# Optimization experiments

Measured on AMD Instinct MI355X. Metric: run time of the kernel, lower is better.

The kernel has to match this reference:

```python
import jax, jax.numpy as jnp
import numpy as np

N_NODES = 16
N_EDGES = 64
N_LAYERS = 4


def _gcn(x, src, dst, emask, W, b):
    # PyG GCNConv: add self-loops, symmetric deg^-1/2 normalization, sum-aggregate.
    n = x.shape[0]
    h = x @ W  # [n, d_out]
    deg = jax.ops.segment_sum(emask, dst, num_segments=n) + 1.0  # +1 self-loop
    dinv = jax.lax.rsqrt(deg)
    norm = dinv[src] * dinv[dst] * emask  # masked-out edges get 0 weight
    out = jax.ops.segment_sum(norm[:, None] * h[src], dst, num_segments=n)
    return out + (dinv * dinv)[:, None] * h + b  # self-loop term + bias


def _sag_pool(x, src, dst, emask, w_rel, b_rel, w_root, k):
    # SAGPooling with GraphConv scorer: score = lin_rel(sum_j x_j) + lin_root(x)
    n = x.shape[0]
    agg = jax.ops.segment_sum(emask[:, None] * x[src], dst, num_segments=n)
    score = agg @ w_rel + b_rel + x @ w_root  # [n]
    perm = jnp.argsort(-score)[:k]  # top-k nodes
    x_new = x[perm] * jnp.tanh(score[perm])[:, None]
    kept = jnp.zeros(n, bool).at[perm].set(True)
    pos = jnp.zeros(n, jnp.int32).at[perm].set(jnp.arange(k, dtype=jnp.int32))
    emask_new = emask * kept[src] * kept[dst]  # drop edges touching removed nodes
    return x_new, pos[src], pos[dst], emask_new


def _conv_gnn(x, src, dst, W0, Ws, bs, pWrel, pbrel, pWroot, linW, linb):
    emask = jnp.ones(src.shape[0], x.dtype)
    n = x.shape[0]
    for i in range(N_LAYERS):
        W = W0 if i == 0 else Ws[i - 1]
        x = jax.nn.relu(_gcn(x, src, dst, emask, W, bs[i]))
        k = -(-n // 2)  # ceil(0.5 * n) -- SAGPooling ratio=0.5
        x, src, dst, emask = _sag_pool(x, src, dst, emask, pWrel[i], pbrel[i], pWroot[i], k)
        n = k
    x = x @ linW + linb  # [1, 128]
    return jax.nn.log_softmax(x, axis=1)


def _fc(h, fcW, fcb, lnw, lnb):
    eps = 1e-5
    for i in range(3):
        h = h @ fcW[i] + fcb[i]
        mu = h.mean(-1, keepdims=True)
        var = ((h - mu) ** 2).mean(-1, keepdims=True)
        h = (h - mu) * jax.lax.rsqrt(var + eps) * lnw[i] + lnb[i]
        h = jax.nn.relu(h)
    return h @ fcW[3] + fcb[3]


def setup_inputs() -> dict:
    key = jax.random.key(0)
    ks = iter(jax.random.split(key, 64))

    def rn(shape, s=0.05):
        return jax.random.normal(next(ks), shape, jnp.float32) * s

    def gnn_params(p):
        return {
            p + '_W0': rn((45, 128)), p + '_W': rn((3, 128, 128)),
            p + '_b': jnp.zeros((4, 128), jnp.float32),
            p + '_pWrel': rn((4, 128)), p + '_pbrel': jnp.zeros((4,), jnp.float32),
            p + '_pWroot': rn((4, 128)),
            p + '_linW': rn((128, 128)), p + '_linb': jnp.zeros((128,), jnp.float32),
        }

    inp = {
        'gp_x': rn((N_NODES, 45), 1.0), 'sp_x': rn((N_NODES, 45), 1.0),
        'gp_src': jax.random.randint(next(ks), (N_EDGES,), 0, N_NODES, jnp.int32),
        'gp_dst': jax.random.randint(next(ks), (N_EDGES,), 0, N_NODES, jnp.int32),
        'sp_src': jax.random.randint(next(ks), (N_EDGES,), 0, N_NODES, jnp.int32),
        'sp_dst': jax.random.randint(next(ks), (N_EDGES,), 0, N_NODES, jnp.int32),
        'fcW': rn((4, 256, 256)), 'fcb': jnp.zeros((4, 256), jnp.float32),
        'lnw': jnp.ones((3, 256), jnp.float32), 'lnb': jnp.zeros((3, 256), jnp.float32),
    }
    inp.update(gnn_params('g'))
    inp.update(gnn_params('s'))
    return inp


def reference(gp_x, sp_x, gp_src, gp_dst, sp_src, sp_dst,
              g_W0, g_W, g_b, g_pWrel, g_pbrel, g_pWroot, g_linW, g_linb,
              s_W0, s_W, s_b, s_pWrel, s_pbrel, s_pWroot, s_linW, s_linb,
              fcW, fcb, lnw, lnb):
    out1 = _conv_gnn(gp_x, gp_src, gp_dst, g_W0, g_W, g_b, g_pWrel, g_pbrel, g_pWroot, g_linW, g_linb)
    out2 = _conv_gnn(sp_x, sp_src, sp_dst, s_W0, s_W, s_b, s_pWrel, s_pbrel, s_pWroot, s_linW, s_linb)
    concat = jnp.concatenate((out1.reshape(-1), out2.reshape(-1)))  # [256]
    return _fc(concat, fcW, fcb, lnw, lnb)
```

## Files before the change

### kernel.cpp

```cpp
#include <hip/hip_runtime.h>
#include <math.h>

#define MAGIC 0x5F3759DFu
typedef unsigned int u32;

__device__ __forceinline__ void bar_lds(){
  asm volatile("s_waitcnt lgkmcnt(0)\n\ts_barrier" ::: "memory");
}
__device__ __forceinline__ void bar_vm0(){
  asm volatile("s_waitcnt vmcnt(0) lgkmcnt(0)\n\ts_barrier" ::: "memory");
}
__device__ __forceinline__ void bar_vm8(){
  asm volatile("s_waitcnt vmcnt(8) lgkmcnt(0)\n\ts_barrier" ::: "memory");
}

__device__ inline float wsum(float v){
  #pragma unroll
  for (int o=32;o;o>>=1) v += __shfl_xor(v,o,64);
  return v;
}
__device__ inline float wmax(float v){
  #pragma unroll
  for (int o=32;o;o>>=1) v = fmaxf(v,__shfl_xor(v,o,64));
  return v;
}
__device__ inline float hsum32(float v){
  #pragma unroll
  for (int o=16;o;o>>=1) v += __shfl_xor(v,o,64);
  return v;
}
__device__ __forceinline__ void stageW(const float* g, float* l, int nfloats,
                                       int wid, int lane){
  const int nch = nfloats>>8;
  for (int c=wid; c<nch; c+=8)
    __builtin_amdgcn_global_load_lds(
      (__attribute__((address_space(1))) u32*)(void*)(g+(c<<8)+(lane<<2)),
      (__attribute__((address_space(3))) u32*)(void*)(l+(c<<8)), 16, 0, 0);
}
__device__ __forceinline__ void pf(const float* p, int nfloats, int tid){
  float4 acc={0.f,0.f,0.f,0.f};
  const int nq=nfloats>>2;
  for (int i=tid;i<nq;i+=512){
    const float4 v=((const float4*)p)[i];
    acc.x+=v.x; acc.y+=v.y; acc.z+=v.z; acc.w+=v.w;
  }
  asm volatile("" :: "v"(acc.x),"v"(acc.y),"v"(acc.z),"v"(acc.w));
}
__device__ __forceinline__ void poll1(const u32* f, int lane){
  u32 v=0;
  do {
    if (lane==0) v=__hip_atomic_load(f,__ATOMIC_ACQUIRE,__HIP_MEMORY_SCOPE_AGENT);
    v=(u32)__shfl((int)v,0,64);
    if (v!=MAGIC) __builtin_amdgcn_s_sleep(1);
  } while (v!=MAGIC);
}
__device__ __forceinline__ float aload(const float* p){
  return __hip_atomic_load(p,__ATOMIC_RELAXED,__HIP_MEMORY_SCOPE_AGENT);
}
__device__ __forceinline__ void astore(float* p, float v){
  __hip_atomic_store(p,v,__ATOMIC_RELAXED,__HIP_MEMORY_SCOPE_AGENT);
}

template<int F,int VH,int N>
__device__ __forceinline__ void cmain2(int lt, const float* slot,
                                       const float* ZBp, float* PBp){
  constexpr int CH = 128/F;
  const int c4 = lt&31, r = lt>>5;
  const int fh = r & (F-1), vh = r / F;
  const int f0 = fh*CH;
  const float4* slot4 = (const float4*)slot;
  float4 acc[VH];
  #pragma unroll
  for (int i=0;i<VH;++i) acc[i]=make_float4(0.f,0.f,0.f,0.f);
  #pragma unroll
  for (int f=0; f<CH; ++f){
    const float4 w4 = slot4[(f0+f)*32 + c4];
    #pragma unroll
    for (int i=0;i<VH;++i){
      const float zv = ZBp[((vh*VH+i)<<7) + f0 + f];
      acc[i].x+=zv*w4.x; acc[i].y+=zv*w4.y; acc[i].z+=zv*w4.z; acc[i].w+=zv*w4.w;
    }
  }
  #pragma unroll
  for (int i=0;i<VH;++i){
    acc[i].x+=__shfl_xor(acc[i].x,32,64);
    acc[i].y+=__shfl_xor(acc[i].y,32,64);
    acc[i].z+=__shfl_xor(acc[i].z,32,64);
    acc[i].w+=__shfl_xor(acc[i].w,32,64);
  }
  if (!(r&1)){
    const int fp = fh>>1;
    float4* P4=(float4*)PBp;
    #pragma unroll
    for (int i=0;i<VH;++i)
      P4[(fp*N + vh*VH + i)*32 + c4] = acc[i];
  }
}

__global__ __launch_bounds__(512,1) void net_kernel(
    const float* __restrict__ gp_x, const float* __restrict__ sp_x,
    const int* __restrict__ gp_src, const int* __restrict__ gp_dst,
    const int* __restrict__ sp_src, const int* __restrict__ sp_dst,
    const float* __restrict__ g_W0, const float* __restrict__ g_W,
    const float* __restrict__ g_b,  const float* __restrict__ g_pWrel,
    const float* __restrict__ g_pbrel, const float* __restrict__ g_pWroot,
    const float* __restrict__ g_linW, const float* __restrict__ g_linb,
    const float* __restrict__ s_W0, const float* __restrict__ s_W,
    const float* __restrict__ s_b,  const float* __restrict__ s_pWrel,
    const float* __restrict__ s_pbrel, const float* __restrict__ s_pWroot,
    const float* __restrict__ s_linW, const float* __restrict__ s_linb,
    const float* __restrict__ fcW, const float* __restrict__ fcb,
    const float* __restrict__ lnw, const float* __restrict__ lnb,
    float* __restrict__ wsbuf, float* __restrict__ out)
{
  __shared__ __align__(16) float slotA[16384];
  __shared__ __align__(16) float slotB[16384];
  __shared__ __align__(16) float XBx[16][128];
  __shared__ __align__(16) float ZBraw[1024];
  __shared__ __align__(16) float PBf[2048];
  __shared__ __align__(16) float wrelL[512], wrootL[512];
  __shared__ __align__(16) float Adn[256], Mdn[256];
  __shared__ float d1P[64], d2P[64];
  __shared__ float yA[128];
  __shared__ float tsA[8]; __shared__ int permA[8];
  __shared__ float fcin[256]; __shared__ float wpart[16];
  __shared__ int   cntL[16];

  const int lt  = threadIdx.x;
  const int bid = blockIdx.x;
  const int wid = lt>>6, lane = lt&63;
  const int qfc = (wid<<3)+(lane&7);

  if (bid >= 5){
    if (bid==5){ pf(g_W0,5760,lt); pf(g_pWrel,512,lt); pf(g_pWroot,512,lt);
                 pf(g_b,512,lt);   pf(g_linb,128,lt); }
    else if (bid==6){ pf(s_W0,5760,lt); pf(s_pWrel,512,lt); pf(s_pWroot,512,lt);
                 pf(s_b,512,lt);   pf(s_linb,128,lt); }
    else if (bid<=10) pf(g_W + (bid-7)*12288, 12288, lt);
    else if (bid<=14) pf(s_W + (bid-11)*12288, 12288, lt);
    else if (bid<=16) pf(g_linW + (bid-15)*8192, 8192, lt);
    else              pf(s_linW + (bid-17)*8192, 8192, lt);
    return;
  }

  if (bid >= 2){
    const int L = bid-1;
    const int f0fc=(lane>>3)<<5;
    float4 wr[32];
    #pragma unroll
    for (int t=0;t<32;++t) wr[t]=*(const float4*)(fcW+(L<<16)+(f0fc+t)*256+(qfc<<2));
    const float4 bb=*(const float4*)(fcb+(L<<8)+(qfc<<2));
    float4 lw={0,0,0,0}, lb2={0,0,0,0};
    if (L<3){ lw=*(const float4*)(lnw+(L<<8)+(qfc<<2)); lb2=*(const float4*)(lnb+(L<<8)+(qfc<<2)); }

    float zr[32];
    if (bid==2){
      float b0=0.f,w0=0.f,l0=0.f;
      if (lt<256){ b0=fcb[lt]; w0=lnw[lt]; l0=lnb[lt]; }
      poll1((const u32*)(wsbuf+256), lane);
      poll1((const u32*)(wsbuf+576), lane);
      float h=0.f;
      if (lt<256){
        h = aload(wsbuf+lt) + aload(wsbuf+320+lt) + b0;
        float s=wsum(h), s2=wsum(h*h);
        if (lane==0){ wpart[wid]=s; wpart[8+wid]=s2; }
      }
      bar_lds();
      if (lt<256){
        const float S =wpart[0]+wpart[1]+wpart[2]+wpart[3];
        const float S2=wpart[8]+wpart[9]+wpart[10]+wpart[11];
        const float mu=S*(1.f/256.f);
        const float ri=rsqrtf(S2*(1.f/256.f)-mu*mu+1e-5f);
        fcin[lt]=fmaxf((h-mu)*ri*w0+l0,0.f);
      }
      bar_lds();
      #pragma unroll
      for (int t=0;t<32;++t) zr[t]=fcin[f0fc+t];
    } else {
      const int floff = (bid==3)?896:1216;
      const int srcoff= (bid==3)?640:960;
      poll1((const u32*)(wsbuf+floff), lane);
      #pragma unroll
      for (int t=0;t<32;++t) zr[t]=aload(wsbuf+srcoff+f0fc+t);
    }
    float4 a={0.f,0.f,0.f,0.f};
    #pragma unroll
    for (int t=0;t<32;++t){
      a.x+=zr[t]*wr[t].x; a.y+=zr[t]*wr[t].y; a.z+=zr[t]*wr[t].z; a.w+=zr[t]*wr[t].w;
    }
    #pragma unroll
    for (int m=8;m<64;m<<=1){
      a.x+=__shfl_xor(a.x,m,64); a.y+=__shfl_xor(a.y,m,64);
      a.z+=__shfl_xor(a.z,m,64); a.w+=__shfl_xor(a.w,m,64);
    }
    if (bid==4){
      if (lane<8){
        float4 r; r.x=a.x+bb.x; r.y=a.y+bb.y; r.z=a.z+bb.z; r.w=a.w+bb.w;
        *(float4*)(out+(qfc<<2))=r;
      }
      return;
    }
    const bool act=(lane<8);
    float4 hv={0.f,0.f,0.f,0.f};
    if (act){
      hv.x=a.x+bb.x; hv.y=a.y+bb.y; hv.z=a.z+bb.z; hv.w=a.w+bb.w;
      float s=hv.x+hv.y+hv.z+hv.w;
      float s2=hv.x*hv.x+hv.y*hv.y+hv.z*hv.z+hv.w*hv.w;
      #pragma unroll
      for (int m=1;m<8;m<<=1){ s+=__shfl_xor(s,m,64); s2+=__shfl_xor(s2,m,64); }
      if (lane==0){ wpart[wid]=s; wpart[8+wid]=s2; }
    }
    bar_lds();
    if (act){
      float S=0.f,S2=0.f;
      #pragma unroll
      for (int w2=0;w2<8;++w2){ S+=wpart[w2]; S2+=wpart[8+w2]; }
      const float mu=S*(1.f/256.f);
      const float ri=rsqrtf(S2*(1.f/256.f)-mu*mu+1e-5f);
      float* dst=wsbuf + ((bid==2)?640:960) + (qfc<<2);
      astore(dst+0,fmaxf((hv.x-mu)*ri*lw.x+lb2.x,0.f));
      astore(dst+1,fmaxf((hv.y-mu)*ri*lw.y+lb2.y,0.f));
      astore(dst+2,fmaxf((hv.z-mu)*ri*lw.z+lb2.z,0.f));
      astore(dst+3,fmaxf((hv.w-mu)*ri*lw.w+lb2.w,0.f));
    }
    bar_vm0();
    if (lt==0) __hip_atomic_store((u32*)(wsbuf+((bid==2)?896:1216)),MAGIC,__ATOMIC_RELEASE,__HIP_MEMORY_SCOPE_AGENT);
    return;
  }

  const int br = bid;
  const float* x0    = br ? sp_x    : gp_x;
  const int*   srcg  = br ? sp_src  : gp_src;
  const int*   dstg  = br ? sp_dst  : gp_dst;
  const float* W0    = br ? s_W0    : g_W0;
  const float* Wl    = br ? s_W     : g_W;
  const float* bl    = br ? s_b     : g_b;
  const float* wrel  = br ? s_pWrel : g_pWrel;
  const float* brel  = br ? s_pbrel : g_pbrel;
  const float* wroot = br ? s_pWroot: g_pWroot;
  const float* linWg = br ? s_linW  : g_linW;
  const float* linb  = br ? s_linb  : g_linb;
  float* wsOut = wsbuf + br*320;
  u32*   wsFlag = (u32*)(wsbuf + 256 + br*320);
  const int f0fc=(lane>>3)<<4;

  float xv[4];
  #pragma unroll
  for (int r=0;r<4;++r){
    const int i=lt+(r<<9), v=i>>7, f=i&127;
    xv[r] = (f<45)? x0[v*45+f] : 0.f;
  }
  int es=0, ed=0; float emk=0.f;
  if (lt<64){ es=srcg[lt]; ed=dstg[lt]; emk=1.f; }
  const float4 brelv = *(const float4*)brel;
  const int bi4=(lt&31)<<2;
  const float4 blv0=*(const float4*)(bl       + bi4);
  const float4 blv1=*(const float4*)(bl + 128 + bi4);
  const float4 blv2=*(const float4*)(bl + 256 + bi4);
  const float4 blv3=*(const float4*)(bl + 384 + bi4);
  const float linb_s = linb[lt>>2];
  asm volatile("" ::: "memory");
  stageW(wrel,  wrelL,  512, wid, lane);
  stageW(wroot, wrootL, 512, wid, lane);
  stageW(Wl,    slotA, 16384, wid, lane);

  auto build_dense=[&](int kk, float wlane, bool with_ts){
    const float4 z4={0.f,0.f,0.f,0.f};
    *(float4*)&Adn[lt<<2]=z4;
    *(float4*)&Mdn[lt<<2]=z4;
    if (lt<16) cntL[lt]=0;
    const bool act=(emk!=0.f);
    if (act) atomicAdd(&cntL[ed],1);
    const float dinvl = (lt<16)? rsqrtf(1.f+(float)cntL[lt]) : 0.f;
    const float dvs=__shfl(dinvl,es,64);
    const float dvd=__shfl(dinvl,ed,64);
    if (act){
      atomicAdd(&Adn[ed*16+es], dvs*dvd*wlane);
      atomicAdd(&Mdn[ed*16+es], 1.f);
    }
    if (lt<kk){
      const float tv = with_ts ? tsA[lt] : 1.f;
      atomicAdd(&Adn[lt*17], dinvl*dinvl*tv);
    }
  };
  auto doE=[&](int n,int k,float bv,bool rebuild){
    if (lt<64){
      float sc=-INFINITY;
      if (lt<n){
        float acc=d2P[lt<<2]+bv;
        for (int u=0;u<n;++u) acc += Mdn[lt*16+u]*d1P[u<<2];
        sc=acc;
      }
      int rank=0;
      for (int u=0;u<n;++u){
        const float su=__shfl(sc,u,64);
        rank += (su>sc || (su==sc && u<lt)) ? 1:0;
      }
      const int kept=(lt<n && rank<k)?1:0;
      const int pos=kept?rank:0;
      const float tval=kept?tanhf(sc):0.f;
      if (kept){ permA[rank]=lt; tsA[rank]=tval; }
      const float ts_src=__shfl(tval,es,64);
      const int ks=__shfl(kept,es,64), kd=__shfl(kept,ed,64);
      const int ps=__shfl(pos,es,64),  pd=__shfl(pos,ed,64);
      emk *= (float)(ks&kd);
      es=ps; ed=pd;
      if (rebuild) build_dense(k, ts_src, true);
    }
  };
  auto doB=[&](int n){
    if (lt<(n<<5)){
      const int v=lt>>5, j4=(lt&31)<<2;
      float4 a={0.f,0.f,0.f,0.f};
      for (int u=0;u<n;++u){
        const float w=Adn[v*16+u];
        const float4 xs=*(const float4*)&XBx[permA[u]][j4];
        a.x+=w*xs.x; a.y+=w*xs.y; a.z+=w*xs.z; a.w+=w*xs.w;
      }
      *(float4*)&ZBraw[(v<<7)+j4]=a;
    }
  };
  auto creduce2=[&](int F, int N, int L, float4 bl4){
    if (lt < (N<<5)){
      const int v=lt>>5, c4=lt&31;
      const float4* P4=(const float4*)PBf;
      float4 acc=bl4;
      for (int fp=0; fp<(F>>1); ++fp){
        const float4 p=P4[(fp*N+v)*32+c4];
        acc.x+=p.x; acc.y+=p.y; acc.z+=p.z; acc.w+=p.w;
      }
      float4 o;
      o.x=fmaxf(acc.x,0.f); o.y=fmaxf(acc.y,0.f);
      o.z=fmaxf(acc.z,0.f); o.w=fmaxf(acc.w,0.f);
      *(float4*)&XBx[v][c4<<2]=o;
      const float4 wr4=*(const float4*)&wrelL[(L<<7)+(c4<<2)];
      const float4 wo4=*(const float4*)&wrootL[(L<<7)+(c4<<2)];
      float p1=o.x*wr4.x+o.y*wr4.y+o.z*wr4.z+o.w*wr4.w;
      float p2=o.x*wo4.x+o.y*wo4.y+o.z*wo4.z+o.w*wo4.w;
      p1=hsum32(p1); p2=hsum32(p2);
      if ((lane&31)==0){ d1P[v<<2]=p1; d2P[v<<2]=p2; }
    }
  };

  #pragma unroll
  for (int r=0;r<4;++r){
    const int i=lt+(r<<9), v=i>>7, f=i&127;
    XBx[v][f]=xv[r];
  }
  if (lt<64) build_dense(16, 1.f, false);
  bar_lds();

  if (lt<256){
    const int v=lt>>4, j4=(lt&15)<<2;
    if (j4<48){
      float4 a={0.f,0.f,0.f,0.f};
      for (int u=0;u<16;++u){
        const float w=Adn[v*16+u];
        const float4 xs=*(const float4*)&XBx[u][j4];
        a.x+=w*xs.x; a.y+=w*xs.y; a.z+=w*xs.z; a.w+=w*xs.w;
      }
      *(float4*)&ZBraw[v*48+j4]=a;
    }
  }
  bar_vm8();

  {
    const int v=lt>>5, c4=lt&31, j4=c4<<2;
    const float* zrow=&ZBraw[v*48];
    float4 a={0.f,0.f,0.f,0.f};
    #pragma unroll
    for (int bb=0;bb<2;++bb){
      float4 wr[16]; float zr[16];
      #pragma unroll
      for (int t=0;t<16;++t){ wr[t]=*(const float4*)(W0+(bb*16+t)*128+j4); zr[t]=zrow[bb*16+t]; }
      #pragma unroll
      for (int t=0;t<16;++t){ a.x+=zr[t]*wr[t].x; a.y+=zr[t]*wr[t].y; a.z+=zr[t]*wr[t].z; a.w+=zr[t]*wr[t].w; }
    }
    { float4 wr[13]; float zr[13];
      #pragma unroll
      for (int t=0;t<13;++t){ wr[t]=*(const float4*)(W0+(32+t)*128+j4); zr[t]=zrow[32+t]; }
      #pragma unroll
      for (int t=0;t<13;++t){ a.x+=zr[t]*wr[t].x; a.y+=zr[t]*wr[t].y; a.z+=zr[t]*wr[t].z; a.w+=zr[t]*wr[t].w; }
    }
    float4 ox;
    ox.x=fmaxf(a.x+blv0.x,0.f); ox.y=fmaxf(a.y+blv0.y,0.f);
    ox.z=fmaxf(a.z+blv0.z,0.f); ox.w=fmaxf(a.w+blv0.w,0.f);
    *(float4*)&XBx[v][j4]=ox;
    const float4 wr4=*(const float4*)&wrelL[j4];
    const float4 wo4=*(const float4*)&wrootL[j4];
    float p1=ox.x*wr4.x+ox.y*wr4.y+ox.z*wr4.z+ox.w*wr4.w;
    float p2=ox.x*wo4.x+ox.y*wo4.y+ox.z*wo4.z+ox.w*wo4.w;
    p1=hsum32(p1); p2=hsum32(p2);
    if ((lane&31)==0){
      const int vv=(wid<<1)|(lane>>5);
      d1P[vv<<2]=p1; d2P[vv<<2]=p2;
    }
  }
  float4 wfc[16];
  #pragma unroll
  for (int t=0;t<16;++t)
    wfc[t]=*(const float4*)(fcW + ((br<<7)+f0fc+t)*256 + (qfc<<2));
  asm volatile("" ::: "memory");
  stageW(Wl+16384, slotB, 16384, wid, lane);
  float4 csum={0.f,0.f,0.f,0.f};
  #pragma unroll
  for (int t=0;t<16;++t){ csum.x+=wfc[t].x; csum.y+=wfc[t].y; csum.z+=wfc[t].z; csum.w+=wfc[t].w; }
  bar_lds();

  doE(16, 8, brelv.x, true);    bar_lds();
  doB(8);                       bar_vm8();
  cmain2<4,2,8>(lt, slotA, ZBraw, PBf);  bar_lds();
  creduce2(4, 8, 1, blv1);      bar_lds();
  stageW(Wl+32768, slotA, 16384, wid, lane);
  doE(8, 4, brelv.y, true);     bar_lds();
  doB(4);                       bar_vm8();
  cmain2<8,2,4>(lt, slotB, ZBraw, PBf); bar_lds();
  creduce2(8, 4, 2, blv2);      bar_lds();
  stageW(linWg, slotB, 16384, wid, lane);
  doE(4, 2, brelv.z, true);     bar_lds();
  doB(2);                       bar_vm8();
  cmain2<8,1,2>(lt, slotA, ZBraw, PBf); bar_lds();
  creduce2(8, 2, 3, blv3);      bar_vm0();

  {
    const float bv=brelv.w;
    const float s0v = d2P[0]+bv + Mdn[0] *d1P[0] + Mdn[1] *d1P[4];
    const float s1v = d2P[4]+bv + Mdn[16]*d1P[0] + Mdn[17]*d1P[4];
    const int   prow = (s1v>s0v) ? 1 : 0;
    const float tsf  = tanhf(prow ? s1v : s0v);
    const int oj=lt>>2, fh=lt&3;
    float p=0.f;
    #pragma unroll
    for (int i=0;i<32;++i){
      const int f=(fh<<5)+i;
      p += XBx[prow][f]*slotB[f*128+oj];
    }
    p+=__shfl_xor(p,1,64); p+=__shfl_xor(p,2,64);
    if (fh==0) yA[oj]=p*tsf+linb_s;
  }
  bar_lds();
  {
    const float a0=yA[lane], b0=yA[64+lane];
    const float m=wmax(fmaxf(a0,b0));
    const float sum=wsum(expf(a0-m)+expf(b0-m));
    const float lse=m+logf(sum);
    float4 a={0.f,0.f,0.f,0.f};
    #pragma unroll
    for (int t=0;t<16;++t){
      const float zv=yA[f0fc+t];
      a.x+=zv*wfc[t].x; a.y+=zv*wfc[t].y; a.z+=zv*wfc[t].z; a.w+=zv*wfc[t].w;
    }
    float4 cs=csum;
    #pragma unroll
    for (int m2=8;m2<64;m2<<=1){
      a.x+=__shfl_xor(a.x,m2,64); a.y+=__shfl_xor(a.y,m2,64);
      a.z+=__shfl_xor(a.z,m2,64); a.w+=__shfl_xor(a.w,m2,64);
      cs.x+=__shfl_xor(cs.x,m2,64); cs.y+=__shfl_xor(cs.y,m2,64);
      cs.z+=__shfl_xor(cs.z,m2,64); cs.w+=__shfl_xor(cs.w,m2,64);
    }
    if (lane<8){
      float* dst=wsOut+(qfc<<2);
      astore(dst+0, a.x - lse*cs.x);
      astore(dst+1, a.y - lse*cs.y);
      astore(dst+2, a.z - lse*cs.z);
      astore(dst+3, a.w - lse*cs.w);
    }
  }
  bar_vm0();
  if (lt==0) __hip_atomic_store(wsFlag, MAGIC, __ATOMIC_RELEASE, __HIP_MEMORY_SCOPE_AGENT);
}

extern "C" void kernel_launch(void* const* d_in, const int* in_sizes, int n_in,
                              void* d_out, int out_size, void* d_ws, size_t ws_size,
                              hipStream_t stream){
  net_kernel<<<19,512,0,stream>>>(
    (const float*)d_in[0],(const float*)d_in[1],
    (const int*)d_in[2],(const int*)d_in[3],(const int*)d_in[4],(const int*)d_in[5],
    (const float*)d_in[10],(const float*)d_in[11],(const float*)d_in[12],(const float*)d_in[13],
    (const float*)d_in[14],(const float*)d_in[15],(const float*)d_in[16],(const float*)d_in[17],
    (const float*)d_in[18],(const float*)d_in[19],(const float*)d_in[20],(const float*)d_in[21],
    (const float*)d_in[22],(const float*)d_in[23],(const float*)d_in[24],(const float*)d_in[25],
    (const float*)d_in[6],(const float*)d_in[7],(const float*)d_in[8],(const float*)d_in[9],
    (float*)d_ws,(float*)d_out);
}
```

Baseline: 23.72 us.

## Reorder GCN to transform-then-aggregate, fusing aggregation into partial reduction

```diff
diff --git a/kernel.cpp b/kernel.cpp
--- a/kernel.cpp
+++ b/kernel.cpp
@@ -62,13 +62,17 @@
 }
 
 template<int F,int VH,int N>
-__device__ __forceinline__ void cmain2(int lt, const float* slot,
-                                       const float* ZBp, float* PBp){
+__device__ __forceinline__ void cmainp(int lt, const float* slot,
+                                       const float* Xp, const int* perm,
+                                       float* PBp){
   constexpr int CH = 128/F;
   const int c4 = lt&31, r = lt>>5;
   const int fh = r & (F-1), vh = r / F;
   const int f0 = fh*CH;
   const float4* slot4 = (const float4*)slot;
+  int ro[VH];
+  #pragma unroll
+  for (int i=0;i<VH;++i) ro[i] = perm[vh*VH+i]<<7;
   float4 acc[VH];
   #pragma unroll
   for (int i=0;i<VH;++i) acc[i]=make_float4(0.f,0.f,0.f,0.f);
@@ -77,7 +81,7 @@
     const float4 w4 = slot4[(f0+f)*32 + c4];
     #pragma unroll
     for (int i=0;i<VH;++i){
-      const float zv = ZBp[((vh*VH+i)<<7) + f0 + f];
+      const float zv = Xp[ro[i]+f0+f];
       acc[i].x+=zv*w4.x; acc[i].y+=zv*w4.y; acc[i].z+=zv*w4.z; acc[i].w+=zv*w4.w;
     }
   }
@@ -116,7 +120,6 @@
   __shared__ __align__(16) float slotA[16384];
   __shared__ __align__(16) float slotB[16384];
   __shared__ __align__(16) float XBx[16][128];
-  __shared__ __align__(16) float ZBraw[1024];
   __shared__ __align__(16) float PBf[2048];
   __shared__ __align__(16) float wrelL[512], wrootL[512];
   __shared__ __align__(16) float Adn[256], Mdn[256];
@@ -125,6 +128,7 @@
   __shared__ float tsA[8]; __shared__ int permA[8];
   __shared__ float fcin[256]; __shared__ float wpart[16];
   __shared__ int   cntL[16];
+  __shared__ int   idPerm[16];
 
   const int lt  = threadIdx.x;
   const int bid = blockIdx.x;
@@ -308,30 +312,23 @@
       if (rebuild) build_dense(k, ts_src, true);
     }
   };
-  auto doB=[&](int n){
-    if (lt<(n<<5)){
-      const int v=lt>>5, j4=(lt&31)<<2;
-      float4 a={0.f,0.f,0.f,0.f};
-      for (int u=0;u<n;++u){
-        const float w=Adn[v*16+u];
-        const float4 xs=*(const float4*)&XBx[permA[u]][j4];
-        a.x+=w*xs.x; a.y+=w*xs.y; a.z+=w*xs.z; a.w+=w*xs.w;
-      }
-      *(float4*)&ZBraw[(v<<7)+j4]=a;
-    }
-  };
-  auto creduce2=[&](int F, int N, int L, float4 bl4){
+  auto bagg=[&](int FH, int N, int L, float4 bl4){
     if (lt < (N<<5)){
       const int v=lt>>5, c4=lt&31;
       const float4* P4=(const float4*)PBf;
-      float4 acc=bl4;
-      for (int fp=0; fp<(F>>1); ++fp){
-        const float4 p=P4[(fp*N+v)*32+c4];
-        acc.x+=p.x; acc.y+=p.y; acc.z+=p.z; acc.w+=p.w;
+      float4 z=bl4;
+      for (int u=0;u<N;++u){
+        float4 t=P4[(u<<5)+c4];
+        for (int fp=1; fp<FH; ++fp){
+          const float4 p=P4[(fp*N+u)*32+c4];
+          t.x+=p.x; t.y+=p.y; t.z+=p.z; t.w+=p.w;
+        }
+        const float a=Adn[v*16+u];
+        z.x+=a*t.x; z.y+=a*t.y; z.z+=a*t.z; z.w+=a*t.w;
       }
       float4 o;
-      o.x=fmaxf(acc.x,0.f); o.y=fmaxf(acc.y,0.f);
-      o.z=fmaxf(acc.z,0.f); o.w=fmaxf(acc.w,0.f);
+      o.x=fmaxf(z.x,0.f); o.y=fmaxf(z.y,0.f);
+      o.z=fmaxf(z.z,0.f); o.w=fmaxf(z.w,0.f);
       *(float4*)&XBx[v][c4<<2]=o;
       const float4 wr4=*(const float4*)&wrelL[(L<<7)+(c4<<2)];
       const float4 wo4=*(const float4*)&wrootL[(L<<7)+(c4<<2)];
@@ -350,51 +347,25 @@
   if (lt<64) build_dense(16, 1.f, false);
   bar_lds();
 
-  if (lt<256){
-    const int v=lt>>4, j4=(lt&15)<<2;
-    if (j4<48){
-      float4 a={0.f,0.f,0.f,0.f};
-      for (int u=0;u<16;++u){
-        const float w=Adn[v*16+u];
-        const float4 xs=*(const float4*)&XBx[u][j4];
-        a.x+=w*xs.x; a.y+=w*xs.y; a.z+=w*xs.z; a.w+=w*xs.w;
-      }
-      *(float4*)&ZBraw[v*48+j4]=a;
-    }
-  }
-  bar_vm8();
-
   {
     const int v=lt>>5, c4=lt&31, j4=c4<<2;
-    const float* zrow=&ZBraw[v*48];
+    const float* xr=&XBx[v][0];
     float4 a={0.f,0.f,0.f,0.f};
     #pragma unroll
     for (int bb=0;bb<2;++bb){
       float4 wr[16]; float zr[16];
       #pragma unroll
-      for (int t=0;t<16;++t){ wr[t]=*(const float4*)(W0+(bb*16+t)*128+j4); zr[t]=zrow[bb*16+t]; }
+      for (int t=0;t<16;++t){ wr[t]=*(const float4*)(W0+(bb*16+t)*128+j4); zr[t]=xr[bb*16+t]; }
       #pragma unroll
       for (int t=0;t<16;++t){ a.x+=zr[t]*wr[t].x; a.y+=zr[t]*wr[t].y; a.z+=zr[t]*wr[t].z; a.w+=zr[t]*wr[t].w; }
     }
     { float4 wr[13]; float zr[13];
       #pragma unroll
-      for (int t=0;t<13;++t){ wr[t]=*(const float4*)(W0+(32+t)*128+j4); zr[t]=zrow[32+t]; }
+      for (int t=0;t<13;++t){ wr[t]=*(const float4*)(W0+(32+t)*128+j4); zr[t]=xr[32+t]; }
       #pragma unroll
       for (int t=0;t<13;++t){ a.x+=zr[t]*wr[t].x; a.y+=zr[t]*wr[t].y; a.z+=zr[t]*wr[t].z; a.w+=zr[t]*wr[t].w; }
     }
-    float4 ox;
-    ox.x=fmaxf(a.x+blv0.x,0.f); ox.y=fmaxf(a.y+blv0.y,0.f);
-    ox.z=fmaxf(a.z+blv0.z,0.f); ox.w=fmaxf(a.w+blv0.w,0.f);
-    *(float4*)&XBx[v][j4]=ox;
-    const float4 wr4=*(const float4*)&wrelL[j4];
-    const float4 wo4=*(const float4*)&wrootL[j4];
-    float p1=ox.x*wr4.x+ox.y*wr4.y+ox.z*wr4.z+ox.w*wr4.w;
-    float p2=ox.x*wo4.x+ox.y*wo4.y+ox.z*wo4.z+ox.w*wo4.w;
-    p1=hsum32(p1); p2=hsum32(p2);
-    if ((lane&31)==0){
-      const int vv=(wid<<1)|(lane>>5);
-      d1P[vv<<2]=p1; d2P[vv<<2]=p2;
-    }
+    *(float4*)&PBf[(v<<7)+j4]=a;
   }
   float4 wfc[16];
   #pragma unroll
@@ -407,20 +378,18 @@
   for (int t=0;t<16;++t){ csum.x+=wfc[t].x; csum.y+=wfc[t].y; csum.z+=wfc[t].z; csum.w+=wfc[t].w; }
   bar_lds();
 
-  doE(16, 8, brelv.x, true);    bar_lds();
-  doB(8);                       bar_vm8();
-  cmain2<4,2,8>(lt, slotA, ZBraw, PBf);  bar_lds();
-  creduce2(4, 8, 1, blv1);      bar_lds();
+  bagg(1, 16, 0, blv0);          bar_lds();
+  doE(16, 8, brelv.x, true);     bar_lds();
+  cmainp<4,2,8>(lt, slotA, &XBx[0][0], permA, PBf);  bar_lds();
   stageW(Wl+32768, slotA, 16384, wid, lane);
-  doE(8, 4, brelv.y, true);     bar_lds();
-  doB(4);                       bar_vm8();
-  cmain2<8,2,4>(lt, slotB, ZBraw, PBf); bar_lds();
-  creduce2(8, 4, 2, blv2);      bar_lds();
+  bagg(2, 8, 1, blv1);           bar_lds();
+  doE(8, 4, brelv.y, true);      bar_vm8();
+  cmainp<8,2,4>(lt, slotB, &XBx[0][0], permA, PBf);  bar_lds();
   stageW(linWg, slotB, 16384, wid, lane);
-  doE(4, 2, brelv.z, true);     bar_lds();
-  doB(2);                       bar_vm8();
-  cmain2<8,1,2>(lt, slotA, ZBraw, PBf); bar_lds();
-  creduce2(8, 2, 3, blv3);      bar_vm0();
+  bagg(4, 4, 2, blv2);           bar_lds();
+  doE(4, 2, brelv.z, true);      bar_vm8();
+  cmainp<8,1,2>(lt, slotA, &XBx[0][0], permA, PBf);  bar_lds();
+  bagg(4, 2, 3, blv3);           bar_vm0();
 
   {
     const float bv=brelv.w;
```

New measurement: 24.45 us. 1.03x slower.
